# Performance work log

Hardware: AMD Instinct MI355X
Metric: run time of the kernel (lower is better)

The kernel has to match this reference:

```python
import jax, jax.numpy as jnp
import numpy as np

NEG_INF = np.finfo(np.float32).min


def setup_inputs() -> dict:
    key = jax.random.key(0)
    ks = jax.random.split(key, 7)
    N, K, H = 30000, 32, 128
    return {
        "h_V": jax.random.normal(ks[0], (N, H), jnp.float32),
        "h_E": jax.random.normal(ks[1], (N, K, H), jnp.float32),
        "mask_attend": jax.random.randint(ks[2], (N, K), 0, 2, jnp.int32),
        "W_Q": jax.random.normal(ks[3], (H, H), jnp.float32) * (1.0 / np.sqrt(H)),
        "W_K": jax.random.normal(ks[4], (H, H), jnp.float32) * (1.0 / np.sqrt(H)),
        "W_V": jax.random.normal(ks[5], (H, H), jnp.float32) * (1.0 / np.sqrt(H)),
        "W_O": jax.random.normal(ks[6], (H, H), jnp.float32) * (1.0 / np.sqrt(H)),
    }


def reference(h_V, h_E, mask_attend, W_Q, W_K, W_V, W_O):
    n_heads = 4
    N, K, Hd = h_E.shape
    d = Hd // n_heads
    # nn.Linear(bias=False): y = x @ W.T
    Q = (h_V @ W_Q.T).reshape(N, n_heads, d)          # [N, h, d]
    Kk = (h_E @ W_K.T).reshape(N, K, n_heads, d)      # [N, K, h, d]
    V = (h_E @ W_V.T).reshape(N, K, n_heads, d)       # [N, K, h, d]
    logits = jnp.einsum('nhd,nkhd->nhk', Q, Kk) / np.float32(np.sqrt(d))  # [N, h, K]
    mask = mask_attend.astype(logits.dtype)[:, None, :]                   # [N, 1, K]
    logits = jnp.where(mask > 0, logits, jnp.float32(NEG_INF))
    attend = jax.nn.softmax(logits, axis=-1) * mask                       # [N, h, K]
    out = jnp.einsum('nhk,nkhd->nhd', attend, V).reshape(N, Hd)
    return out @ W_O.T
```

## Files before the change

### kernel.cpp

```cpp
#include <hip/hip_runtime.h>
#include <hip/hip_bf16.h>

#define NEG_INF (-3.402823466e+38f)
#define SCALE 0.17677669529663689f

typedef __attribute__((ext_vector_type(8))) short bf16x8;
typedef __attribute__((ext_vector_type(4))) float f32x4;
typedef __attribute__((ext_vector_type(4))) unsigned short u16x4;
typedef __attribute__((ext_vector_type(4))) unsigned int u32x4;

__device__ __forceinline__ unsigned short f2bf(float f) {
  union { float f; unsigned u; } v; v.f = f;
  unsigned r = v.u + 0x7fffu + ((v.u >> 16) & 1u);
  return (unsigned short)(r >> 16);
}

__device__ __forceinline__ unsigned pack2(float lo, float hi) {
  __hip_bfloat162 h2 = __float22bfloat162_rn(make_float2(lo, hi));
  return *reinterpret_cast<unsigned*>(&h2);
}

__device__ __forceinline__ bf16x8 pack_bf8(const float* __restrict__ p) {
  float4 a = *(const float4*)p;
  float4 b = *(const float4*)(p + 4);
  u32x4 u;
  u[0] = pack2(a.x, a.y); u[1] = pack2(a.z, a.w);
  u[2] = pack2(b.x, b.y); u[3] = pack2(b.z, b.w);
  return __builtin_bit_cast(bf16x8, u);
}

__global__ __launch_bounds__(256) void fuse_weights(
    const float* __restrict__ wq, const float* __restrict__ wk,
    const float* __restrict__ wv, const float* __restrict__ wo,
    unsigned short* __restrict__ MT, unsigned short* __restrict__ WB) {
  const int w = (blockIdx.x * 256 + threadIdx.x) >> 6;
  const int lane = threadIdx.x & 63;
  const int lr = lane & 15, lk = lane >> 4;
  const int h = w >> 6, t2 = w & 63, jt = t2 >> 3, it = t2 & 7;

  bf16x8 a, b;
#pragma unroll
  for (int j = 0; j < 8; ++j) {
    a[j] = (short)f2bf(wq[(h * 32 + lk * 8 + j) * 128 + jt * 16 + lr]);
    b[j] = (short)f2bf(wk[(h * 32 + lk * 8 + j) * 128 + it * 16 + lr]);
  }
  f32x4 c = (f32x4){0.f, 0.f, 0.f, 0.f};
  c = __builtin_amdgcn_mfma_f32_16x16x32_bf16(a, b, c, 0, 0, 0);
#pragma unroll
  for (int r = 0; r < 4; ++r)
    MT[h * 16384 + (it * 16 + lr) * 128 + jt * 16 + lk * 4 + r] = f2bf(c[r]);

  bf16x8 a2 = pack_bf8(wo + (jt * 16 + lr) * 128 + h * 32 + lk * 8);
  bf16x8 b2;
#pragma unroll
  for (int j = 0; j < 8; ++j)
    b2[j] = (short)f2bf(wv[(h * 32 + lk * 8 + j) * 128 + it * 16 + lr]);
  f32x4 c2 = (f32x4){0.f, 0.f, 0.f, 0.f};
  c2 = __builtin_amdgcn_mfma_f32_16x16x32_bf16(a2, b2, c2, 0, 0, 0);
#pragma unroll
  for (int r = 0; r < 4; ++r)
    WB[(size_t)(jt * 16 + lk * 4 + r) * 512 + h * 128 + it * 16 + lr] = f2bf(c2[r]);
}

__global__ __launch_bounds__(256) void gemm_wq(
    const float* __restrict__ X, const unsigned short* __restrict__ MT,
    unsigned short* __restrict__ WQb, int M) {
  __shared__ unsigned short Wl[128 * 136];
  const int wave = threadIdx.x >> 6, lane = threadIdx.x & 63;
  const int lr = lane & 15, lk = lane >> 4;
  const int row0 = blockIdx.x * 64 + wave * 16;
  const int arow = row0 + lr;

  bf16x8 af[4];
  if (arow < M) {
    const float* xr = X + (size_t)arow * 128;
#pragma unroll
    for (int kk = 0; kk < 4; ++kk) af[kk] = pack_bf8(xr + kk * 32 + lk * 8);
  } else {
#pragma unroll
    for (int kk = 0; kk < 4; ++kk) af[kk] = (bf16x8)(short)0;
  }

  for (int h = 0; h < 4; ++h) {
    __syncthreads();
    const unsigned short* Wsrc = MT + (size_t)h * 16384;
    for (int idx = threadIdx.x; idx < 2048; idx += 256) {
      int row = idx >> 4, col = (idx & 15) * 8;
      *(bf16x8*)&Wl[row * 136 + col] = *(const bf16x8*)(Wsrc + row * 128 + col);
    }
    __syncthreads();

    f32x4 acc[8];
#pragma unroll
    for (int ct = 0; ct < 8; ++ct) acc[ct] = (f32x4){0.f, 0.f, 0.f, 0.f};
#pragma unroll
    for (int kk = 0; kk < 4; ++kk)
#pragma unroll
      for (int ct = 0; ct < 8; ++ct) {
        bf16x8 b = *(const bf16x8*)&Wl[(ct * 16 + lr) * 136 + kk * 32 + lk * 8];
        acc[ct] = __builtin_amdgcn_mfma_f32_16x16x32_bf16(af[kk], b, acc[ct], 0, 0, 0);
      }

#pragma unroll
    for (int ct = 0; ct < 8; ++ct)
#pragma unroll
      for (int r = 0; r < 4; ++r) {
        int row = row0 + lk * 4 + r;
        if (row < M)
          WQb[(size_t)row * 512 + h * 128 + ct * 16 + lr] = f2bf(acc[ct][r]);
      }
  }
}

__global__ __launch_bounds__(256, 4) void neigh_aE(
    const float* __restrict__ hE, const int* __restrict__ mask,
    const unsigned short* __restrict__ WQb, unsigned short* __restrict__ aEb,
    int N) {
  __shared__ unsigned short Elds[4][32 * 128];
  __shared__ unsigned short attL[4][128];

  const int wave = threadIdx.x >> 6, lane = threadIdx.x & 63;
  const int lr = lane & 15, lk = lane >> 4;
  unsigned short* El = Elds[wave];
  unsigned short* at = attL[wave];
  const int n = blockIdx.x * 4 + wave;
  if (n >= N) return;

  const int4 m0 = *(const int4*)(mask + (size_t)n * 32 + lk * 4);
  const int4 m1 = *(const int4*)(mask + (size_t)n * 32 + 16 + lk * 4);
  const int mrow0 = mask[(size_t)n * 32 + lr];
  const int mrow1 = mask[(size_t)n * 32 + 16 + lr];

  const float* E = hE + (size_t)n * 4096;
  const float4 z4 = make_float4(0.f, 0.f, 0.f, 0.f);
  float4 raw[16];
#pragma unroll
  for (int q = 0; q < 8; ++q) {
    const bool live = (q >> 2) ? (mrow1 != 0) : (mrow0 != 0);
    const float* p = E + ((q >> 2) * 16 + lr) * 128 + (q & 3) * 32 + lk * 8;
    if (live) {
      raw[q * 2] = *(const float4*)p;
      raw[q * 2 + 1] = *(const float4*)(p + 4);
    } else {
      raw[q * 2] = z4;
      raw[q * 2 + 1] = z4;
    }
  }
  bf16x8 bq[4];
#pragma unroll
  for (int kk = 0; kk < 4; ++kk)
    bq[kk] = *(const bf16x8*)(WQb + (size_t)n * 512 + (lr & 3) * 128 + kk * 32 + lk * 8);

  bf16x8 af[2][4];
#pragma unroll
  for (int q = 0; q < 8; ++q) {
    float4 a = raw[q * 2], b = raw[q * 2 + 1];
    u32x4 u;
    u[0] = pack2(a.x, a.y); u[1] = pack2(a.z, a.w);
    u[2] = pack2(b.x, b.y); u[3] = pack2(b.z, b.w);
    bf16x8 t = __builtin_bit_cast(bf16x8, u);
    af[q >> 2][q & 3] = t;
    const int k = (q >> 2) * 16 + lr;
    const int bswz = ((q & 3) * 4 + lk) ^ ((((q >> 2) * 2 + (lr >> 3)) & 3) << 1);
    *(bf16x8*)&El[k * 128 + bswz * 8] = t;
  }

  f32x4 c0 = (f32x4){0.f, 0.f, 0.f, 0.f};
  f32x4 c1 = (f32x4){0.f, 0.f, 0.f, 0.f};
#pragma unroll
  for (int kk = 0; kk < 4; ++kk) {
    c0 = __builtin_amdgcn_mfma_f32_16x16x32_bf16(af[0][kk], bq[kk], c0, 0, 0, 0);
    c1 = __builtin_amdgcn_mfma_f32_16x16x32_bf16(af[1][kk], bq[kk], c1, 0, 0, 0);
  }

  float l[2][4];
  l[0][0] = m0.x ? c0[0] * SCALE : NEG_INF;
  l[0][1] = m0.y ? c0[1] * SCALE : NEG_INF;
  l[0][2] = m0.z ? c0[2] * SCALE : NEG_INF;
  l[0][3] = m0.w ? c0[3] * SCALE : NEG_INF;
  l[1][0] = m1.x ? c1[0] * SCALE : NEG_INF;
  l[1][1] = m1.y ? c1[1] * SCALE : NEG_INF;
  l[1][2] = m1.z ? c1[2] * SCALE : NEG_INF;
  l[1][3] = m1.w ? c1[3] * SCALE : NEG_INF;

  float mx = l[0][0];
#pragma unroll
  for (int rt = 0; rt < 2; ++rt)
#pragma unroll
    for (int r = 0; r < 4; ++r) mx = fmaxf(mx, l[rt][r]);
  mx = fmaxf(mx, __shfl_xor(mx, 16, 64));
  mx = fmaxf(mx, __shfl_xor(mx, 32, 64));

  float e[2][4];
  float sum = 0.f;
#pragma unroll
  for (int rt = 0; rt < 2; ++rt)
#pragma unroll
    for (int r = 0; r < 4; ++r) { e[rt][r] = __expf(l[rt][r] - mx); sum += e[rt][r]; }
  sum += __shfl_xor(sum, 16, 64);
  sum += __shfl_xor(sum, 32, 64);
  const float inv = 1.0f / sum;

  if (lr < 4) {
    u16x4 p0, p1;
    p0[0] = f2bf(m0.x ? e[0][0] * inv : 0.f);
    p0[1] = f2bf(m0.y ? e[0][1] * inv : 0.f);
    p0[2] = f2bf(m0.z ? e[0][2] * inv : 0.f);
    p0[3] = f2bf(m0.w ? e[0][3] * inv : 0.f);
    p1[0] = f2bf(m1.x ? e[1][0] * inv : 0.f);
    p1[1] = f2bf(m1.y ? e[1][1] * inv : 0.f);
    p1[2] = f2bf(m1.z ? e[1][2] * inv : 0.f);
    p1[3] = f2bf(m1.w ? e[1][3] * inv : 0.f);
    *(u16x4*)&at[lr * 32 + lk * 4] = p0;
    *(u16x4*)&at[lr * 32 + 16 + lk * 4] = p1;
  }

  bf16x8 attA = *(const bf16x8*)&at[(lr & 3) * 32 + lk * 8];
  const int e0 = lr & 7;
#pragma unroll
  for (int ct = 0; ct < 8; ++ct) {
    const int blk = (ct * 2 + (lr >> 3)) ^ (lk << 1);
    bf16x8 bE;
#pragma unroll
    for (int j = 0; j < 8; ++j)
      bE[j] = (short)El[(lk * 8 + j) * 128 + blk * 8 + e0];
    f32x4 acc = (f32x4){0.f, 0.f, 0.f, 0.f};
    acc = __builtin_amdgcn_mfma_f32_16x16x32_bf16(attA, bE, acc, 0, 0, 0);
    float v = (lk == 0) ? acc[0] : (lk == 1) ? acc[1] : (lk == 2) ? acc[2] : acc[3];
    aEb[(size_t)n * 512 + lk * 128 + ct * 16 + lr] = f2bf(v);
  }
}

__global__ __launch_bounds__(256) void gemm_out(
    const unsigned short* __restrict__ aEb, const unsigned short* __restrict__ WB,
    float* __restrict__ Y, int M) {
  __shared__ unsigned short Wl[128 * 136];
  const int wave = threadIdx.x >> 6, lane = threadIdx.x & 63;
  const int lr = lane & 15, lk = lane >> 4;
  const int row0 = blockIdx.x * 64 + wave * 16;
  const int arow = row0 + lr;

  f32x4 acc[8];
#pragma unroll
  for (int ct = 0; ct < 8; ++ct) acc[ct] = (f32x4){0.f, 0.f, 0.f, 0.f};

  for (int h = 0; h < 4; ++h) {
    __syncthreads();
    for (int idx = threadIdx.x; idx < 2048; idx += 256) {
      int row = idx >> 4, col = (idx & 15) * 8;
      *(bf16x8*)&Wl[row * 136 + col] = *(const bf16x8*)(WB + (size_t)row * 512 + h * 128 + col);
    }
    __syncthreads();

    bf16x8 af[4];
    if (arow < M) {
#pragma unroll
      for (int kk = 0; kk < 4; ++kk)
        af[kk] = *(const bf16x8*)(aEb + (size_t)arow * 512 + h * 128 + kk * 32 + lk * 8);
    } else {
#pragma unroll
      for (int kk = 0; kk < 4; ++kk) af[kk] = (bf16x8)(short)0;
    }
#pragma unroll
    for (int kk = 0; kk < 4; ++kk)
#pragma unroll
      for (int ct = 0; ct < 8; ++ct) {
        bf16x8 b = *(const bf16x8*)&Wl[(ct * 16 + lr) * 136 + kk * 32 + lk * 8];
        acc[ct] = __builtin_amdgcn_mfma_f32_16x16x32_bf16(af[kk], b, acc[ct], 0, 0, 0);
      }
  }

#pragma unroll
  for (int ct = 0; ct < 8; ++ct)
#pragma unroll
    for (int r = 0; r < 4; ++r) {
      int row = row0 + lk * 4 + r;
      if (row < M) Y[(size_t)row * 128 + ct * 16 + lr] = acc[ct][r];
    }
}

extern "C" void kernel_launch(void* const* d_in, const int* in_sizes, int n_in,
                              void* d_out, int out_size, void* d_ws, size_t ws_size,
                              hipStream_t stream) {
  const float* hV = (const float*)d_in[0];
  const float* hE = (const float*)d_in[1];
  const int* mask = (const int*)d_in[2];
  const float* Wq = (const float*)d_in[3];
  const float* Wk = (const float*)d_in[4];
  const float* Wv = (const float*)d_in[5];
  const float* Wo = (const float*)d_in[6];
  float* out = (float*)d_out;
  const int N = in_sizes[0] / 128;

  char* ws = (char*)d_ws;
  unsigned short* MT = (unsigned short*)(ws);
  unsigned short* WB = (unsigned short*)(ws + 131072);
  unsigned short* WQb = (unsigned short*)(ws + 262144);
  unsigned short* aEb = (unsigned short*)(ws + 262144 + (size_t)N * 1024);

  fuse_weights<<<64, 256, 0, stream>>>(Wq, Wk, Wv, Wo, MT, WB);
  gemm_wq<<<(N + 63) / 64, 256, 0, stream>>>(hV, MT, WQb, N);
  neigh_aE<<<(N + 3) / 4, 256, 0, stream>>>(hE, mask, WQb, aEb, N);
  gemm_out<<<(N + 63) / 64, 256, 0, stream>>>(aEb, WB, out, N);
}
```

Measured before the change: 124.4 us.

## Fuse output projection into neighbor attention kernel to drop the intermediate buffer

Merges the gemm_out kernel into neigh_aE. Each block now keeps its four rows of aggregated attention output in shared memory, synchronizes, and multiplies them by the fused output weight matrix read directly from global memory. This removes the bf16 intermediate write and re-read through HBM and one kernel launch. In exchange, every 4-row block re-reads the full 128x512 weight matrix from cache. The 16-row MFMA tiles also carry only four useful rows, which adds L2 traffic and wasted matrix work.

```diff
diff --git a/kernel.cpp b/kernel.cpp
--- a/kernel.cpp
+++ b/kernel.cpp
@@ -114,169 +114,152 @@
 
 __global__ __launch_bounds__(256, 4) void neigh_aE(
     const float* __restrict__ hE, const int* __restrict__ mask,
-    const unsigned short* __restrict__ WQb, unsigned short* __restrict__ aEb,
-    int N) {
+    const unsigned short* __restrict__ WQb, const unsigned short* __restrict__ WB,
+    float* __restrict__ out, int N) {
   __shared__ unsigned short Elds[4][32 * 128];
   __shared__ unsigned short attL[4][128];
+  __shared__ unsigned short aEL[4 * 520];
 
   const int wave = threadIdx.x >> 6, lane = threadIdx.x & 63;
   const int lr = lane & 15, lk = lane >> 4;
   unsigned short* El = Elds[wave];
   unsigned short* at = attL[wave];
-  const int n = blockIdx.x * 4 + wave;
-  if (n >= N) return;
-
-  const int4 m0 = *(const int4*)(mask + (size_t)n * 32 + lk * 4);
-  const int4 m1 = *(const int4*)(mask + (size_t)n * 32 + 16 + lk * 4);
-  const int mrow0 = mask[(size_t)n * 32 + lr];
-  const int mrow1 = mask[(size_t)n * 32 + 16 + lr];
-
-  const float* E = hE + (size_t)n * 4096;
-  const float4 z4 = make_float4(0.f, 0.f, 0.f, 0.f);
-  float4 raw[16];
-#pragma unroll
-  for (int q = 0; q < 8; ++q) {
-    const bool live = (q >> 2) ? (mrow1 != 0) : (mrow0 != 0);
-    const float* p = E + ((q >> 2) * 16 + lr) * 128 + (q & 3) * 32 + lk * 8;
-    if (live) {
-      raw[q * 2] = *(const float4*)p;
-      raw[q * 2 + 1] = *(const float4*)(p + 4);
-    } else {
-      raw[q * 2] = z4;
-      raw[q * 2 + 1] = z4;
-    }
-  }
-  bf16x8 bq[4];
-#pragma unroll
-  for (int kk = 0; kk < 4; ++kk)
-    bq[kk] = *(const bf16x8*)(WQb + (size_t)n * 512 + (lr & 3) * 128 + kk * 32 + lk * 8);
-
-  bf16x8 af[2][4];
-#pragma unroll
-  for (int q = 0; q < 8; ++q) {
-    float4 a = raw[q * 2], b = raw[q * 2 + 1];
-    u32x4 u;
-    u[0] = pack2(a.x, a.y); u[1] = pack2(a.z, a.w);
-    u[2] = pack2(b.x, b.y); u[3] = pack2(b.z, b.w);
-    bf16x8 t = __builtin_bit_cast(bf16x8, u);
-    af[q >> 2][q & 3] = t;
-    const int k = (q >> 2) * 16 + lr;
-    const int bswz = ((q & 3) * 4 + lk) ^ ((((q >> 2) * 2 + (lr >> 3)) & 3) << 1);
-    *(bf16x8*)&El[k * 128 + bswz * 8] = t;
-  }
-
-  f32x4 c0 = (f32x4){0.f, 0.f, 0.f, 0.f};
-  f32x4 c1 = (f32x4){0.f, 0.f, 0.f, 0.f};
-#pragma unroll
-  for (int kk = 0; kk < 4; ++kk) {
-    c0 = __builtin_amdgcn_mfma_f32_16x16x32_bf16(af[0][kk], bq[kk], c0, 0, 0, 0);
-    c1 = __builtin_amdgcn_mfma_f32_16x16x32_bf16(af[1][kk], bq[kk], c1, 0, 0, 0);
-  }
-
-  float l[2][4];
-  l[0][0] = m0.x ? c0[0] * SCALE : NEG_INF;
-  l[0][1] = m0.y ? c0[1] * SCALE : NEG_INF;
-  l[0][2] = m0.z ? c0[2] * SCALE : NEG_INF;
-  l[0][3] = m0.w ? c0[3] * SCALE : NEG_INF;
-  l[1][0] = m1.x ? c1[0] * SCALE : NEG_INF;
-  l[1][1] = m1.y ? c1[1] * SCALE : NEG_INF;
-  l[1][2] = m1.z ? c1[2] * SCALE : NEG_INF;
-  l[1][3] = m1.w ? c1[3] * SCALE : NEG_INF;
-
-  float mx = l[0][0];
-#pragma unroll
-  for (int rt = 0; rt < 2; ++rt)
-#pragma unroll
-    for (int r = 0; r < 4; ++r) mx = fmaxf(mx, l[rt][r]);
-  mx = fmaxf(mx, __shfl_xor(mx, 16, 64));
-  mx = fmaxf(mx, __shfl_xor(mx, 32, 64));
-
-  float e[2][4];
-  float sum = 0.f;
-#pragma unroll
-  for (int rt = 0; rt < 2; ++rt)
-#pragma unroll
-    for (int r = 0; r < 4; ++r) { e[rt][r] = __expf(l[rt][r] - mx); sum += e[rt][r]; }
-  sum += __shfl_xor(sum, 16, 64);
-  sum += __shfl_xor(sum, 32, 64);
-  const float inv = 1.0f / sum;
-
-  if (lr < 4) {
-    u16x4 p0, p1;
-    p0[0] = f2bf(m0.x ? e[0][0] * inv : 0.f);
-    p0[1] = f2bf(m0.y ? e[0][1] * inv : 0.f);
-    p0[2] = f2bf(m0.z ? e[0][2] * inv : 0.f);
-    p0[3] = f2bf(m0.w ? e[0][3] * inv : 0.f);
-    p1[0] = f2bf(m1.x ? e[1][0] * inv : 0.f);
-    p1[1] = f2bf(m1.y ? e[1][1] * inv : 0.f);
-    p1[2] = f2bf(m1.z ? e[1][2] * inv : 0.f);
-    p1[3] = f2bf(m1.w ? e[1][3] * inv : 0.f);
-    *(u16x4*)&at[lr * 32 + lk * 4] = p0;
-    *(u16x4*)&at[lr * 32 + 16 + lk * 4] = p1;
-  }
-
-  bf16x8 attA = *(const bf16x8*)&at[(lr & 3) * 32 + lk * 8];
-  const int e0 = lr & 7;
-#pragma unroll
-  for (int ct = 0; ct < 8; ++ct) {
-    const int blk = (ct * 2 + (lr >> 3)) ^ (lk << 1);
-    bf16x8 bE;
-#pragma unroll
-    for (int j = 0; j < 8; ++j)
-      bE[j] = (short)El[(lk * 8 + j) * 128 + blk * 8 + e0];
-    f32x4 acc = (f32x4){0.f, 0.f, 0.f, 0.f};
-    acc = __builtin_amdgcn_mfma_f32_16x16x32_bf16(attA, bE, acc, 0, 0, 0);
-    float v = (lk == 0) ? acc[0] : (lk == 1) ? acc[1] : (lk == 2) ? acc[2] : acc[3];
-    aEb[(size_t)n * 512 + lk * 128 + ct * 16 + lr] = f2bf(v);
-  }
-}
-
-__global__ __launch_bounds__(256) void gemm_out(
-    const unsigned short* __restrict__ aEb, const unsigned short* __restrict__ WB,
-    float* __restrict__ Y, int M) {
-  __shared__ unsigned short Wl[128 * 136];
-  const int wave = threadIdx.x >> 6, lane = threadIdx.x & 63;
-  const int lr = lane & 15, lk = lane >> 4;
-  const int row0 = blockIdx.x * 64 + wave * 16;
-  const int arow = row0 + lr;
-
-  f32x4 acc[8];
-#pragma unroll
-  for (int ct = 0; ct < 8; ++ct) acc[ct] = (f32x4){0.f, 0.f, 0.f, 0.f};
-
-  for (int h = 0; h < 4; ++h) {
-    __syncthreads();
-    for (int idx = threadIdx.x; idx < 2048; idx += 256) {
-      int row = idx >> 4, col = (idx & 15) * 8;
-      *(bf16x8*)&Wl[row * 136 + col] = *(const bf16x8*)(WB + (size_t)row * 512 + h * 128 + col);
-    }
-    __syncthreads();
-
-    bf16x8 af[4];
-    if (arow < M) {
-#pragma unroll
-      for (int kk = 0; kk < 4; ++kk)
-        af[kk] = *(const bf16x8*)(aEb + (size_t)arow * 512 + h * 128 + kk * 32 + lk * 8);
-    } else {
-#pragma unroll
-      for (int kk = 0; kk < 4; ++kk) af[kk] = (bf16x8)(short)0;
-    }
+  const int n0 = blockIdx.x * 4;
+  const int n = n0 + wave;
+  const bool active = (n < N);
+
+  if (active) {
+    const int4 m0 = *(const int4*)(mask + (size_t)n * 32 + lk * 4);
+    const int4 m1 = *(const int4*)(mask + (size_t)n * 32 + 16 + lk * 4);
+    const int mrow0 = mask[(size_t)n * 32 + lr];
+    const int mrow1 = mask[(size_t)n * 32 + 16 + lr];
+
+    const float* E = hE + (size_t)n * 4096;
+    const float4 z4 = make_float4(0.f, 0.f, 0.f, 0.f);
+    float4 raw[16];
+#pragma unroll
+    for (int q = 0; q < 8; ++q) {
+      const bool live = (q >> 2) ? (mrow1 != 0) : (mrow0 != 0);
+      const float* p = E + ((q >> 2) * 16 + lr) * 128 + (q & 3) * 32 + lk * 8;
+      if (live) {
+        raw[q * 2] = *(const float4*)p;
+        raw[q * 2 + 1] = *(const float4*)(p + 4);
+      } else {
+        raw[q * 2] = z4;
+        raw[q * 2 + 1] = z4;
+      }
+    }
+    bf16x8 bq[4];
 #pragma unroll
     for (int kk = 0; kk < 4; ++kk)
-#pragma unroll
-      for (int ct = 0; ct < 8; ++ct) {
-        bf16x8 b = *(const bf16x8*)&Wl[(ct * 16 + lr) * 136 + kk * 32 + lk * 8];
-        acc[ct] = __builtin_amdgcn_mfma_f32_16x16x32_bf16(af[kk], b, acc[ct], 0, 0, 0);
-      }
-  }
-
-#pragma unroll
-  for (int ct = 0; ct < 8; ++ct)
-#pragma unroll
-    for (int r = 0; r < 4; ++r) {
-      int row = row0 + lk * 4 + r;
-      if (row < M) Y[(size_t)row * 128 + ct * 16 + lr] = acc[ct][r];
-    }
+      bq[kk] = *(const bf16x8*)(WQb + (size_t)n * 512 + (lr & 3) * 128 + kk * 32 + lk * 8);
+
+    bf16x8 af[2][4];
+#pragma unroll
+    for (int q = 0; q < 8; ++q) {
+      float4 a = raw[q * 2], b = raw[q * 2 + 1];
+      u32x4 u;
+      u[0] = pack2(a.x, a.y); u[1] = pack2(a.z, a.w);
+      u[2] = pack2(b.x, b.y); u[3] = pack2(b.z, b.w);
+      bf16x8 t = __builtin_bit_cast(bf16x8, u);
+      af[q >> 2][q & 3] = t;
+      const int k = (q >> 2) * 16 + lr;
+      const int bswz = ((q & 3) * 4 + lk) ^ ((((q >> 2) * 2 + (lr >> 3)) & 3) << 1);
+      *(bf16x8*)&El[k * 128 + bswz * 8] = t;
+    }
+
+    f32x4 c0 = (f32x4){0.f, 0.f, 0.f, 0.f};
+    f32x4 c1 = (f32x4){0.f, 0.f, 0.f, 0.f};
+#pragma unroll
+    for (int kk = 0; kk < 4; ++kk) {
+      c0 = __builtin_amdgcn_mfma_f32_16x16x32_bf16(af[0][kk], bq[kk], c0, 0, 0, 0);
+      c1 = __builtin_amdgcn_mfma_f32_16x16x32_bf16(af[1][kk], bq[kk], c1, 0, 0, 0);
+    }
+
+    float l[2][4];
+    l[0][0] = m0.x ? c0[0] * SCALE : NEG_INF;
+    l[0][1] = m0.y ? c0[1] * SCALE : NEG_INF;
+    l[0][2] = m0.z ? c0[2] * SCALE : NEG_INF;
+    l[0][3] = m0.w ? c0[3] * SCALE : NEG_INF;
+    l[1][0] = m1.x ? c1[0] * SCALE : NEG_INF;
+    l[1][1] = m1.y ? c1[1] * SCALE : NEG_INF;
+    l[1][2] = m1.z ? c1[2] * SCALE : NEG_INF;
+    l[1][3] = m1.w ? c1[3] * SCALE : NEG_INF;
+
+    float mx = l[0][0];
+#pragma unroll
+    for (int rt = 0; rt < 2; ++rt)
+#pragma unroll
+      for (int r = 0; r < 4; ++r) mx = fmaxf(mx, l[rt][r]);
+    mx = fmaxf(mx, __shfl_xor(mx, 16, 64));
+    mx = fmaxf(mx, __shfl_xor(mx, 32, 64));
+
+    float e[2][4];
+    float sum = 0.f;
+#pragma unroll
+    for (int rt = 0; rt < 2; ++rt)
+#pragma unroll
+      for (int r = 0; r < 4; ++r) { e[rt][r] = __expf(l[rt][r] - mx); sum += e[rt][r]; }
+    sum += __shfl_xor(sum, 16, 64);
+    sum += __shfl_xor(sum, 32, 64);
+    const float inv = 1.0f / sum;
+
+    if (lr < 4) {
+      u16x4 p0, p1;
+      p0[0] = f2bf(m0.x ? e[0][0] * inv : 0.f);
+      p0[1] = f2bf(m0.y ? e[0][1] * inv : 0.f);
+      p0[2] = f2bf(m0.z ? e[0][2] * inv : 0.f);
+      p0[3] = f2bf(m0.w ? e[0][3] * inv : 0.f);
+      p1[0] = f2bf(m1.x ? e[1][0] * inv : 0.f);
+      p1[1] = f2bf(m1.y ? e[1][1] * inv : 0.f);
+      p1[2] = f2bf(m1.z ? e[1][2] * inv : 0.f);
+      p1[3] = f2bf(m1.w ? e[1][3] * inv : 0.f);
+      *(u16x4*)&at[lr * 32 + lk * 4] = p0;
+      *(u16x4*)&at[lr * 32 + 16 + lk * 4] = p1;
+    }
+
+    bf16x8 attA = *(const bf16x8*)&at[(lr & 3) * 32 + lk * 8];
+    const int e0 = lr & 7;
+#pragma unroll
+    for (int ct = 0; ct < 8; ++ct) {
+      const int blk = (ct * 2 + (lr >> 3)) ^ (lk << 1);
+      bf16x8 bE;
+#pragma unroll
+      for (int j = 0; j < 8; ++j)
+        bE[j] = (short)El[(lk * 8 + j) * 128 + blk * 8 + e0];
+      f32x4 acc = (f32x4){0.f, 0.f, 0.f, 0.f};
+      acc = __builtin_amdgcn_mfma_f32_16x16x32_bf16(attA, bE, acc, 0, 0, 0);
+      float v = (lk == 0) ? acc[0] : (lk == 1) ? acc[1] : (lk == 2) ? acc[2] : acc[3];
+      aEL[wave * 520 + lk * 128 + ct * 16 + lr] = f2bf(v);
+    }
+  }
+
+  __syncthreads();
+
+  {
+    f32x4 po[2];
+    po[0] = (f32x4){0.f, 0.f, 0.f, 0.f};
+    po[1] = (f32x4){0.f, 0.f, 0.f, 0.f};
+#pragma unroll
+    for (int kk16 = 0; kk16 < 16; ++kk16) {
+      bf16x8 aA = *(const bf16x8*)&aEL[(lr & 3) * 520 + kk16 * 32 + lk * 8];
+#pragma unroll
+      for (int c = 0; c < 2; ++c) {
+        const int ct = wave * 2 + c;
+        bf16x8 b = *(const bf16x8*)(WB + (size_t)(ct * 16 + lr) * 512 + kk16 * 32 + lk * 8);
+        po[c] = __builtin_amdgcn_mfma_f32_16x16x32_bf16(aA, b, po[c], 0, 0, 0);
+      }
+    }
+    if (lk == 0) {
+#pragma unroll
+      for (int c = 0; c < 2; ++c)
+#pragma unroll
+        for (int r = 0; r < 4; ++r) {
+          const int row = n0 + r;
+          if (row < N) out[(size_t)row * 128 + (wave * 2 + c) * 16 + lr] = po[c][r];
+        }
+    }
+  }
 }
 
 extern "C" void kernel_launch(void* const* d_in, const int* in_sizes, int n_in,
@@ -296,10 +279,8 @@
   unsigned short* MT = (unsigned short*)(ws);
   unsigned short* WB = (unsigned short*)(ws + 131072);
   unsigned short* WQb = (unsigned short*)(ws + 262144);
-  unsigned short* aEb = (unsigned short*)(ws + 262144 + (size_t)N * 1024);
 
   fuse_weights<<<64, 256, 0, stream>>>(Wq, Wk, Wv, Wo, MT, WB);
   gemm_wq<<<(N + 63) / 64, 256, 0, stream>>>(hV, MT, WQb, N);
-  neigh_aE<<<(N + 3) / 4, 256, 0, stream>>>(hE, mask, WQb, aEb, N);
-  gemm_out<<<(N + 63) / 64, 256, 0, stream>>>(aEb, WB, out, N);
-}
+  neigh_aE<<<(N + 3) / 4, 256, 0, stream>>>(hE, mask, WQb, WB, out, N);
+}
```

After: 191.5 us. 53.9% more time.
